# Optimization experiments

Hardware: AMD Instinct MI355X
Metric: run time of the kernel (lower is better)

## Reference

```python
import jax, jax.numpy as jnp
import numpy as np

B, N, M, C, G = 8, 1024, 20000, 80, 64
NMS_THR = 0.5
PULL_W = 1.0
PUSH_W = 1.0
EPS = 1e-6


def _rand_boxes(key, shape):
    k1, k2 = jax.random.split(key)
    xy = jax.random.uniform(k1, shape + (2,), minval=0.0, maxval=900.0)
    wh = jax.random.uniform(k2, shape + (2,), minval=8.0, maxval=120.0)
    return jnp.concatenate([xy, xy + wh], axis=-1).astype(jnp.float32)


def setup_inputs() -> dict:
    key = jax.random.key(0)
    ks = jax.random.split(key, 6)
    return {
        "pos_inds": jax.random.randint(ks[0], (B, N), 0, M, dtype=jnp.int32),
        "pos_gt_index": jax.random.randint(ks[1], (B, N), 0, G, dtype=jnp.int32),
        "gt_bboxes": _rand_boxes(ks[2], (B, G)),
        "bbox_preds": _rand_boxes(ks[3], (B, N)),
        "cls_scores": jax.random.uniform(ks[4], (B, M, C), dtype=jnp.float32),
        "gt_labels": jax.random.randint(ks[5], (B, G), 0, C, dtype=jnp.int32),
    }


def pairwise_iou(b1, b2):
    # legacy +1 convention, matching bbox_overlaps(mode='iou')
    lt = jnp.maximum(b1[:, None, :2], b2[None, :, :2])
    rb = jnp.minimum(b1[:, None, 2:], b2[None, :, 2:])
    wh = jnp.clip(rb - lt + 1.0, 0.0)
    ov = wh[..., 0] * wh[..., 1]
    a1 = (b1[:, 2] - b1[:, 0] + 1.0) * (b1[:, 3] - b1[:, 1] + 1.0)
    a2 = (b2[:, 2] - b2[:, 0] + 1.0) * (b2[:, 3] - b2[:, 1] + 1.0)
    return ov / (a1[:, None] + a2[None, :] - ov)


def nms_loss_single(boxes, scores, gt_index, gt_boxes):
    # boxes [N,4], scores [N], gt_index [N] int, gt_boxes [G,4]
    n = boxes.shape[0]
    g_n = gt_boxes.shape[0]
    # push_select=True: first operand of IoU is detached
    iou = pairwise_iou(jax.lax.stop_gradient(boxes), boxes)  # [N,N]
    gtiou = jax.lax.stop_gradient(pairwise_iou(gt_boxes, gt_boxes))  # [G,G]
    s_det = jax.lax.stop_gradient(scores)

    init = (jnp.ones((n,), bool), -jnp.ones((g_n,), jnp.int32),
            jnp.float32(0.0), jnp.float32(0.0), jnp.int32(0), jnp.int32(0))

    def step(carry, _):
        alive, seen, tpull, tpush, pcnt, qcnt = carry
        any_alive = jnp.any(alive)
        i = jnp.argmax(jnp.where(alive, s_det, -jnp.inf))  # pop highest score
        g = gt_index[i]
        prev = seen[g]
        has_seen = (prev >= 0) & any_alive
        # pull: pull_relax=True, use_score=True
        max_s_iou = jnp.maximum(iou[prev, i], EPS)
        pull = jnp.where(has_seen, -jnp.log(1.0 - NMS_THR + max_s_iou) * scores[i], 0.0)
        seen = jnp.where(any_alive & (prev < 0), seen.at[g].set(i.astype(jnp.int32)), seen)
        pcnt = pcnt + has_seen.astype(jnp.int32)
        alive = alive.at[i].set(False)
        remaining = jnp.any(alive)  # torch breaks (dropping this step's pull) if empty
        row = iou[i]
        overlap = alive & (row > NMS_THR)
        push_mask = overlap & (gt_index != g) & (row > gtiou[g, gt_index])
        n_push = jnp.sum(push_mask)
        # push: push_relax=False, use_score=True, scores NOT detached
        terms = -jnp.log(jnp.where(push_mask, 1.0 - row, 1.0)) * scores
        push = jnp.where(n_push > 0,
                         jnp.sum(jnp.where(push_mask, terms, 0.0)) / jnp.maximum(n_push, 1).astype(jnp.float32),
                         0.0)
        add = any_alive & remaining
        tpull = tpull + jnp.where(add, pull, 0.0)
        tpush = tpush + jnp.where(add, push, 0.0)
        qcnt = qcnt + jnp.where(add, n_push.astype(jnp.int32), 0)
        alive = alive & ~overlap
        return (alive, seen, tpull, tpush, pcnt, qcnt), None

    (alive, seen, tpull, tpush, pcnt, qcnt), _ = jax.lax.scan(step, init, None, length=n)
    pull = tpull / (pcnt.astype(jnp.float32) + EPS)
    push = tpush / (qcnt.astype(jnp.float32) + EPS)
    return push, pull


def reference(pos_inds, pos_gt_index, gt_bboxes, bbox_preds, cls_scores, gt_labels):
    labels = jnp.take_along_axis(gt_labels, pos_gt_index, axis=1)            # [B,N]
    sel = jnp.take_along_axis(cls_scores, pos_inds[..., None], axis=1)       # [B,N,C]
    scores = jnp.take_along_axis(sel, labels[..., None].astype(jnp.int32), axis=2)[..., 0]  # [B,N]
    push, pull = jax.vmap(nms_loss_single)(bbox_preds, scores, pos_gt_index, gt_bboxes)
    return jnp.stack([jnp.mean(push) * PUSH_W, jnp.mean(pull) * PULL_W])
```

## Files before the change

### kernel.cpp

```cpp
#include <hip/hip_runtime.h>
#include <math.h>

#define B_ 8
#define N_ 1024
#define M_ 20000
#define C_ 80
#define G_ 64
typedef unsigned long long ull;

#define WS_ELEM_OFF 0
#define WS_ADJ_OFF  262144

__device__ __forceinline__ float iou1(float ax, float ay, float az, float aw,
                                      float bx, float by, float bz, float bw) {
    float lx = fmaxf(ax, bx), ly = fmaxf(ay, by);
    float rx = fminf(az, bz), ry = fminf(aw, bw);
    float w = fmaxf(rx - lx + 1.0f, 0.0f), h = fmaxf(ry - ly + 1.0f, 0.0f);
    float ov = w * h;
    float a1 = (az - ax + 1.0f) * (aw - ay + 1.0f);
    float a2 = (bz - bx + 1.0f) * (bw - by + 1.0f);
    return ov / (a1 + a2 - ov);
}

__global__ __launch_bounds__(1024) void prep_kernel(
    const int* __restrict__ pos_inds, const int* __restrict__ pos_gt,
    const float* __restrict__ bbox_preds, const float* __restrict__ cls_scores,
    const int* __restrict__ gt_labels, float4* __restrict__ elemG) {
    const int b = blockIdx.x, t = threadIdx.x;
    __shared__ ull s_keys[N_];

    int g0 = pos_gt[b * N_ + t];
    int lab = gt_labels[b * G_ + g0];
    int pi = pos_inds[b * N_ + t];
    float s = cls_scores[(size_t)b * (M_ * C_) + (size_t)pi * C_ + lab];
    ull key = ((ull)(~__float_as_uint(s)) << 32) | (unsigned)t;

    for (unsigned k2 = 2; k2 <= N_; k2 <<= 1) {
        for (unsigned jj = k2 >> 1; jj; jj >>= 1) {
            ull other;
            if (jj >= 64) {
                s_keys[t] = key; __syncthreads();
                other = s_keys[t ^ jj]; __syncthreads();
            } else {
                int lo = __shfl_xor((int)(unsigned)key, (int)jj);
                int hi = __shfl_xor((int)(unsigned)(key >> 32), (int)jj);
                other = ((ull)(unsigned)hi << 32) | (unsigned)lo;
            }
            bool keep_min = (((t & jj) == 0) == ((t & k2) == 0));
            ull mn = key < other ? key : other;
            ull mx = key < other ? other : key;
            key = keep_min ? mn : mx;
        }
    }

    int j = (int)(unsigned)(key & 0xFFFFFFFFull);
    float ss = __uint_as_float(~(unsigned)(key >> 32));
    const float* bp = bbox_preds + (size_t)(b * N_ + j) * 4;
    float x0 = bp[0], y0 = bp[1], x1 = bp[2], y1 = bp[3];
    int g = pos_gt[b * N_ + j];
    float area = (x1 - x0 + 1.0f) * (y1 - y0 + 1.0f);
    elemG[(size_t)(b * N_ + t) * 2 + 0] = make_float4(x0, y0, x1, y1);
    elemG[(size_t)(b * N_ + t) * 2 + 1] = make_float4(__int_as_float(g), ss, area, 0.f);
}

__global__ __launch_bounds__(256) void adj_kernel(
    const float4* __restrict__ elemG, unsigned short* __restrict__ adjG) {
    const int b = blockIdx.y;
    const int r = blockIdx.x * 4 + (threadIdx.x >> 6);
    const int lane = threadIdx.x & 63;
    float4 rA = elemG[(size_t)(b * N_ + r) * 2];
    float ax0 = rA.x, ay0 = rA.y;
    float az1 = rA.z + 1.0f, aw1 = rA.w + 1.0f;
    float a1 = (rA.z - rA.x + 1.0f) * (rA.w - rA.y + 1.0f);
    unsigned bits = 0;
#pragma unroll
    for (int u = 0; u < 16; ++u) {
        int cpos = lane * 16 + u;
        float4 cA = elemG[(size_t)(b * N_ + cpos) * 2];
        float lx = fmaxf(ax0, cA.x), ly = fmaxf(ay0, cA.y);
        float rx = fminf(az1, cA.z + 1.0f), ry = fminf(aw1, cA.w + 1.0f);
        float w = fmaxf(rx - lx, 0.0f), h = fmaxf(ry - ly, 0.0f);
        float I = w * h;
        float a2 = (cA.z - cA.x + 1.0f) * (cA.w - cA.y + 1.0f);
        bits |= (3.0f * I > a1 + a2) ? (1u << u) : 0u;
    }
    adjG[(size_t)(b * N_ + r) * 64 + lane] = (unsigned short)bits;
}

__global__ __launch_bounds__(1024) void sweep_loss_kernel(
    const float4* __restrict__ elemG, const unsigned short* __restrict__ adjG,
    const float* __restrict__ gt_bboxes, float* __restrict__ out) {
    const int b = blockIdx.x, t = threadIdx.x;
    const int wtop = t >> 6, lane = t & 63;

    __shared__ float4 s_box[N_];
    __shared__ float s_score[N_];
    __shared__ short s_g[N_];
    __shared__ ull s_S[16];
    __shared__ unsigned short s_step[N_];
    __shared__ unsigned short s_surv[N_];
    __shared__ float s_ts[N_];
    __shared__ int s_cnt[N_], s_kills[N_], s_first[G_];
    __shared__ int s_wpre[17];
    __shared__ float s_tpull, s_tpush;
    __shared__ int s_pcnt, s_qcnt;

    {
        float4 eA = elemG[(size_t)(b * N_ + t) * 2];
        float4 eB = elemG[(size_t)(b * N_ + t) * 2 + 1];
        s_box[t] = eA; s_score[t] = eB.y; s_g[t] = (short)__float_as_int(eB.x);
    }
    s_ts[t] = 0.f; s_cnt[t] = 0; s_kills[t] = 0; s_step[t] = 0xffff;
    if (t < 16) s_S[t] = 0ull;
    if (t < G_) s_first[t] = 0x7fffffff;
    if (t == 0) { s_tpull = 0.f; s_tpush = 0.f; s_pcnt = 0; s_qcnt = 0; }

    const ull* rowp = (const ull*)(adjG + (size_t)(b * N_ + t) * 64);
    ull rw[16];
#pragma unroll
    for (int c = 0; c < 16; ++c) rw[c] = (c <= wtop) ? rowp[c] : 0ull;

    __syncthreads();

    bool alive_f = true;
#pragma unroll
    for (int c = 0; c < 16; ++c) {
        if (wtop == c) {
            ull alive = __ballot(alive_f);
            ull Sc = 0ull;
            const ull below = (1ull << lane) - 1ull;
            const ull myearly = rw[c] & below;
            while (alive) {
                bool inU = ((alive >> lane) & 1ull) && ((myearly & alive) == 0ull);
                ull U = __ballot(inU);
                unsigned klo = inU ? (unsigned)rw[c] : 0u;
                unsigned khi = inU ? (unsigned)(rw[c] >> 32) : 0u;
#pragma unroll
                for (int off = 32; off; off >>= 1) {
                    klo |= (unsigned)__shfl_xor((int)klo, off);
                    khi |= (unsigned)__shfl_xor((int)khi, off);
                }
                ull kills = ((ull)khi << 32) | klo;
                Sc |= U;
                alive &= ~U;
                alive &= ~kills;
            }
            if (lane == 0) s_S[c] = Sc;
        }
        __syncthreads();
        if (wtop > c && alive_f && (rw[c] & s_S[c]) != 0ull) alive_f = false;
    }

    if (t < 16) s_wpre[t + 1] = __popcll(s_S[t]);
    __syncthreads();
    if (t == 0) { s_wpre[0] = 0; for (int w = 0; w < 16; ++w) s_wpre[w + 1] += s_wpre[w]; }
    __syncthreads();
    const int K = s_wpre[16];
    const ull sbit = 1ull << lane;
    const bool isS = (s_S[wtop] & sbit) != 0ull;
    int myrank = -1;
    if (isS) {
        myrank = s_wpre[wtop] + __popcll(s_S[wtop] & (sbit - 1ull));
        s_step[t] = (unsigned short)myrank;
        s_surv[myrank] = (unsigned short)t;
        atomicMin(&s_first[(int)s_g[t]], myrank);
    }
    __syncthreads();

    if (!isS) {
        int kp = -1;
#pragma unroll
        for (int w = 15; w >= 0; --w) {
            ull m = rw[w] & s_S[w];
            if (w == wtop) m &= (1ull << lane) - 1ull;
            if (m) kp = (w << 6) + (int)(__ffsll(m) - 1);
        }
        if (kp >= 0) {
            int q = s_step[kp];
            atomicAdd(&s_kills[q], 1);
            int gq = (int)s_g[kp], gj = (int)s_g[t];
            if (gq != gj) {
                float4 qa = s_box[kp], ja = s_box[t];
                float ov = iou1(qa.x, qa.y, qa.z, qa.w, ja.x, ja.y, ja.z, ja.w);
                const float* gbq = gt_bboxes + (size_t)(b * G_ + gq) * 4;
                const float* gbj = gt_bboxes + (size_t)(b * G_ + gj) * 4;
                float gov = iou1(gbq[0], gbq[1], gbq[2], gbq[3],
                                 gbj[0], gbj[1], gbj[2], gbj[3]);
                if (ov > gov) {
                    atomicAdd(&s_cnt[q], 1);
                    atomicAdd(&s_ts[q], -__logf(1.0f - ov) * s_score[t]);
                }
            }
        }
    }
    __syncthreads();

    if (isS) {
        int k = myrank, g = (int)s_g[t], f = s_first[g];
        if (f < k) {
            atomicAdd(&s_pcnt, 1);
            bool drop = (k == K - 1) && (s_kills[k] == 0);
            if (!drop) {
                float4 fA = s_box[s_surv[f]], kA = s_box[t];
                float ov = iou1(fA.x, fA.y, fA.z, fA.w, kA.x, kA.y, kA.z, kA.w);
                atomicAdd(&s_tpull, -__logf(0.5f + fmaxf(ov, 1e-6f)) * s_score[t]);
            }
        }
        if (s_cnt[k] > 0) {
            atomicAdd(&s_tpush, s_ts[k] / (float)s_cnt[k]);
            atomicAdd(&s_qcnt, s_cnt[k]);
        }
    }
    __syncthreads();

    if (t == 0) {
        atomicAdd(&out[0], (s_tpush / ((float)s_qcnt + 1e-6f)) * 0.125f);
        atomicAdd(&out[1], (s_tpull / ((float)s_pcnt + 1e-6f)) * 0.125f);
    }
}

extern "C" void kernel_launch(void* const* d_in, const int* in_sizes, int n_in,
                              void* d_out, int out_size, void* d_ws, size_t ws_size,
                              hipStream_t stream) {
    const int* pos_inds = (const int*)d_in[0];
    const int* pos_gt = (const int*)d_in[1];
    const float* gt_bboxes = (const float*)d_in[2];
    const float* bbox_preds = (const float*)d_in[3];
    const float* cls_scores = (const float*)d_in[4];
    const int* gt_labels = (const int*)d_in[5];
    float* out = (float*)d_out;

    float4* elemG = (float4*)((char*)d_ws + WS_ELEM_OFF);
    unsigned short* adjG = (unsigned short*)((char*)d_ws + WS_ADJ_OFF);

    hipMemsetAsync(out, 0, 2 * sizeof(float), stream);
    prep_kernel<<<dim3(B_), dim3(1024), 0, stream>>>(
        pos_inds, pos_gt, bbox_preds, cls_scores, gt_labels, elemG);
    adj_kernel<<<dim3(256, B_), dim3(256), 0, stream>>>(elemG, adjG);
    sweep_loss_kernel<<<dim3(B_), dim3(1024), 0, stream>>>(elemG, adjG, gt_bboxes, out);
}
```

Measured before the change: 138.6 us.

## Fuse prep, adjacency and sweep into one per-batch kernel

Merges the sort/gather prep kernel, the pairwise IoU adjacency kernel and the sweep/loss kernel into a single block-per-batch kernel. Sorted boxes and areas are kept in shared memory, and each thread computes its lower-triangular adjacency row bits directly into registers. This removes two kernel launches and the global workspace round trip. In exchange, the adjacency work now runs on only 8 blocks instead of being spread across the whole GPU.

```diff
diff --git a/kernel.cpp b/kernel.cpp
--- a/kernel.cpp
+++ b/kernel.cpp
@@ -7,9 +7,6 @@
 #define C_ 80
 #define G_ 64
 typedef unsigned long long ull;
-
-#define WS_ELEM_OFF 0
-#define WS_ADJ_OFF  262144
 
 __device__ __forceinline__ float iou1(float ax, float ay, float az, float aw,
                                       float bx, float by, float bz, float bw) {
@@ -22,18 +19,43 @@
     return ov / (a1 + a2 - ov);
 }
 
-__global__ __launch_bounds__(1024) void prep_kernel(
+__global__ __launch_bounds__(1024) void nms_fused_kernel(
     const int* __restrict__ pos_inds, const int* __restrict__ pos_gt,
-    const float* __restrict__ bbox_preds, const float* __restrict__ cls_scores,
-    const int* __restrict__ gt_labels, float4* __restrict__ elemG) {
+    const float* __restrict__ gt_bboxes, const float* __restrict__ bbox_preds,
+    const float* __restrict__ cls_scores, const int* __restrict__ gt_labels,
+    float* __restrict__ out) {
     const int b = blockIdx.x, t = threadIdx.x;
+    const int wtop = t >> 6, lane = t & 63;
+
     __shared__ ull s_keys[N_];
-
-    int g0 = pos_gt[b * N_ + t];
-    int lab = gt_labels[b * G_ + g0];
-    int pi = pos_inds[b * N_ + t];
-    float s = cls_scores[(size_t)b * (M_ * C_) + (size_t)pi * C_ + lab];
-    ull key = ((ull)(~__float_as_uint(s)) << 32) | (unsigned)t;
+    __shared__ float4 s_box[N_];
+    __shared__ float s_area[N_];
+    __shared__ float s_score[N_];
+    __shared__ short s_g[N_];
+    __shared__ ull s_S[16];
+    __shared__ unsigned short s_step[N_];
+    __shared__ unsigned short s_surv[N_];
+    __shared__ float s_ts[N_];
+    __shared__ int s_cnt[N_], s_kills[N_];
+    __shared__ int s_first[G_];
+    __shared__ int s_wpre[17];
+    __shared__ float s_tpull, s_tpush;
+    __shared__ int s_pcnt, s_qcnt;
+
+    s_ts[t] = 0.f; s_cnt[t] = 0; s_kills[t] = 0; s_step[t] = 0xffff;
+    if (t < 16) s_S[t] = 0ull;
+    if (t < G_) s_first[t] = 0x7fffffff;
+    if (t == 0) { s_tpull = 0.f; s_tpush = 0.f; s_pcnt = 0; s_qcnt = 0; }
+
+    ull key;
+    {
+        int g0 = pos_gt[b * N_ + t];
+        int lab = gt_labels[b * G_ + g0];
+        int pi = pos_inds[b * N_ + t];
+        float s = cls_scores[(size_t)b * (M_ * C_) + (size_t)pi * C_ + lab];
+        key = ((ull)(~__float_as_uint(s)) << 32) | (unsigned)t;
+    }
+    __syncthreads();
 
     for (unsigned k2 = 2; k2 <= N_; k2 <<= 1) {
         for (unsigned jj = k2 >> 1; jj; jj >>= 1) {
@@ -53,73 +75,40 @@
         }
     }
 
-    int j = (int)(unsigned)(key & 0xFFFFFFFFull);
-    float ss = __uint_as_float(~(unsigned)(key >> 32));
-    const float* bp = bbox_preds + (size_t)(b * N_ + j) * 4;
-    float x0 = bp[0], y0 = bp[1], x1 = bp[2], y1 = bp[3];
-    int g = pos_gt[b * N_ + j];
-    float area = (x1 - x0 + 1.0f) * (y1 - y0 + 1.0f);
-    elemG[(size_t)(b * N_ + t) * 2 + 0] = make_float4(x0, y0, x1, y1);
-    elemG[(size_t)(b * N_ + t) * 2 + 1] = make_float4(__int_as_float(g), ss, area, 0.f);
-}
-
-__global__ __launch_bounds__(256) void adj_kernel(
-    const float4* __restrict__ elemG, unsigned short* __restrict__ adjG) {
-    const int b = blockIdx.y;
-    const int r = blockIdx.x * 4 + (threadIdx.x >> 6);
-    const int lane = threadIdx.x & 63;
-    float4 rA = elemG[(size_t)(b * N_ + r) * 2];
-    float ax0 = rA.x, ay0 = rA.y;
-    float az1 = rA.z + 1.0f, aw1 = rA.w + 1.0f;
-    float a1 = (rA.z - rA.x + 1.0f) * (rA.w - rA.y + 1.0f);
-    unsigned bits = 0;
-#pragma unroll
-    for (int u = 0; u < 16; ++u) {
-        int cpos = lane * 16 + u;
-        float4 cA = elemG[(size_t)(b * N_ + cpos) * 2];
-        float lx = fmaxf(ax0, cA.x), ly = fmaxf(ay0, cA.y);
-        float rx = fminf(az1, cA.z + 1.0f), ry = fminf(aw1, cA.w + 1.0f);
-        float w = fmaxf(rx - lx, 0.0f), h = fmaxf(ry - ly, 0.0f);
-        float I = w * h;
-        float a2 = (cA.z - cA.x + 1.0f) * (cA.w - cA.y + 1.0f);
-        bits |= (3.0f * I > a1 + a2) ? (1u << u) : 0u;
-    }
-    adjG[(size_t)(b * N_ + r) * 64 + lane] = (unsigned short)bits;
-}
-
-__global__ __launch_bounds__(1024) void sweep_loss_kernel(
-    const float4* __restrict__ elemG, const unsigned short* __restrict__ adjG,
-    const float* __restrict__ gt_bboxes, float* __restrict__ out) {
-    const int b = blockIdx.x, t = threadIdx.x;
-    const int wtop = t >> 6, lane = t & 63;
-
-    __shared__ float4 s_box[N_];
-    __shared__ float s_score[N_];
-    __shared__ short s_g[N_];
-    __shared__ ull s_S[16];
-    __shared__ unsigned short s_step[N_];
-    __shared__ unsigned short s_surv[N_];
-    __shared__ float s_ts[N_];
-    __shared__ int s_cnt[N_], s_kills[N_], s_first[G_];
-    __shared__ int s_wpre[17];
-    __shared__ float s_tpull, s_tpush;
-    __shared__ int s_pcnt, s_qcnt;
-
     {
-        float4 eA = elemG[(size_t)(b * N_ + t) * 2];
-        float4 eB = elemG[(size_t)(b * N_ + t) * 2 + 1];
-        s_box[t] = eA; s_score[t] = eB.y; s_g[t] = (short)__float_as_int(eB.x);
-    }
-    s_ts[t] = 0.f; s_cnt[t] = 0; s_kills[t] = 0; s_step[t] = 0xffff;
-    if (t < 16) s_S[t] = 0ull;
-    if (t < G_) s_first[t] = 0x7fffffff;
-    if (t == 0) { s_tpull = 0.f; s_tpush = 0.f; s_pcnt = 0; s_qcnt = 0; }
-
-    const ull* rowp = (const ull*)(adjG + (size_t)(b * N_ + t) * 64);
+        int j = (int)(unsigned)(key & 0xFFFFFFFFull);
+        float ss = __uint_as_float(~(unsigned)(key >> 32));
+        const float* bp = bbox_preds + (size_t)(b * N_ + j) * 4;
+        float x0 = bp[0], y0 = bp[1], x1 = bp[2], y1 = bp[3];
+        s_box[t] = make_float4(x0, y0, x1, y1);
+        s_area[t] = (x1 - x0 + 1.0f) * (y1 - y0 + 1.0f);
+        s_score[t] = ss;
+        s_g[t] = (short)pos_gt[b * N_ + j];
+    }
+    __syncthreads();
+
     ull rw[16];
-#pragma unroll
-    for (int c = 0; c < 16; ++c) rw[c] = (c <= wtop) ? rowp[c] : 0ull;
-
+    {
+        float4 me = s_box[t];
+        float a1 = s_area[t];
+        float ax0 = me.x, ay0 = me.y, az1 = me.z + 1.0f, aw1 = me.w + 1.0f;
+#pragma unroll
+        for (int w = 0; w < 16; ++w) {
+            ull bits = 0ull;
+            if (w <= wtop) {
+                int qbase = w << 6;
+                for (int u = 0; u < 64; ++u) {
+                    float4 o = s_box[qbase + u];
+                    float lx = fmaxf(ax0, o.x), ly = fmaxf(ay0, o.y);
+                    float rx = fminf(az1, o.z + 1.0f), ry = fminf(aw1, o.w + 1.0f);
+                    float ww = fmaxf(rx - lx, 0.0f), hh = fmaxf(ry - ly, 0.0f);
+                    float I = ww * hh;
+                    bits |= (3.0f * I > a1 + s_area[qbase + u]) ? (1ull << u) : 0ull;
+                }
+            }
+            rw[w] = bits;
+        }
+    }
     __syncthreads();
 
     bool alive_f = true;
@@ -230,12 +219,7 @@
     const int* gt_labels = (const int*)d_in[5];
     float* out = (float*)d_out;
 
-    float4* elemG = (float4*)((char*)d_ws + WS_ELEM_OFF);
-    unsigned short* adjG = (unsigned short*)((char*)d_ws + WS_ADJ_OFF);
-
     hipMemsetAsync(out, 0, 2 * sizeof(float), stream);
-    prep_kernel<<<dim3(B_), dim3(1024), 0, stream>>>(
-        pos_inds, pos_gt, bbox_preds, cls_scores, gt_labels, elemG);
-    adj_kernel<<<dim3(256, B_), dim3(256), 0, stream>>>(elemG, adjG);
-    sweep_loss_kernel<<<dim3(B_), dim3(1024), 0, stream>>>(elemG, adjG, gt_bboxes, out);
+    nms_fused_kernel<<<dim3(B_), dim3(1024), 0, stream>>>(
+        pos_inds, pos_gt, gt_bboxes, bbox_preds, cls_scores, gt_labels, out);
 }
```

Result: slower. 196.7 us (+41.9%).
